# Performance work log

Hardware: AMD Instinct MI355X
Metric: run time of the kernel (lower is better)

Reference implementation:

```python
import jax, jax.numpy as jnp
import numpy as np

NUM_TOKENS = 2048
NUM_EXPERTS = 8
TOPK = 2
INTERMEDIATE = 2048
HIDDEN = 1024


def setup_inputs() -> dict:
    key = jax.random.key(0)
    k1, k2, k3 = jax.random.split(key, 3)
    intermediate_states = jax.random.normal(k1, (NUM_TOKENS * TOPK, INTERMEDIATE), dtype=jnp.float32)
    # per-expert down-projection, scaled like a typical init
    w = jax.random.normal(k2, (NUM_EXPERTS, INTERMEDIATE, HIDDEN), dtype=jnp.float32) / np.float32(np.sqrt(INTERMEDIATE))
    router_logits = jax.random.normal(k3, (NUM_TOKENS, NUM_EXPERTS), dtype=jnp.float32)
    return {"intermediate_states": intermediate_states, "w": w, "router_logits": router_logits}


def reference(intermediate_states, w, router_logits):
    T, E = router_logits.shape
    K = TOPK
    H = w.shape[-1]
    # Routing: softmax over experts, then top-k weights/ids (precompute_ctx.full_topk_weight/full_topk_ids)
    probs = jax.nn.softmax(router_logits, axis=-1)          # [T, E]
    topk_w, topk_ids = jax.lax.top_k(probs, K)              # [T, K]
    # Grouped expert GEMM: each (token, k) row is multiplied by its expert's weight.
    # Compute against all experts once, then gather the routed expert per row.
    out_all = jnp.einsum('ri,eih->reh', intermediate_states, w)   # [T*K, E, H]
    flat_ids = topk_ids.reshape(-1)                               # [T*K]
    routed = jnp.take_along_axis(out_all, flat_ids[:, None, None], axis=1)[:, 0, :]  # [T*K, H]
    # topk-weighted reduction over the K expert outputs per token
    out = (routed.reshape(T, K, H) * topk_w[..., None]).sum(axis=1)  # [T, H]
    # reduce-scatter across tensor-parallel ranks: with world_size=1 this is identity
    return out
```

## Files before the change

kernel.cpp:

```cpp
#include <hip/hip_runtime.h>

#define T_TOKENS 2048
#define N_EXPERTS 8
#define ROWS (T_TOKENS * 2)
#define I_DIM 2048
#define H_DIM 1024

#define M_TILE 64
#define N_TILE 128
#define BK 64
#define NSTEP (I_DIM / BK)

#define TP 68

typedef __bf16 bf16x8 __attribute__((ext_vector_type(8)));
typedef float f32x4 __attribute__((ext_vector_type(4)));
typedef unsigned int u32;
typedef u32 u32x4 __attribute__((ext_vector_type(4)));

__device__ inline void load_lds16(const void* g, void* l) {
    __builtin_amdgcn_global_load_lds(
        (const __attribute__((address_space(1))) void*)g,
        (__attribute__((address_space(3))) void*)l, 16, 0, 0);
}

__device__ inline u32 pack2(float a, float b) {
    union { __bf16 h[2]; u32 w; } u;
    u.h[0] = (__bf16)a; u.h[1] = (__bf16)b;
    return u.w;
}

__global__ __launch_bounds__(256) void prep_kernel(
    const float* __restrict__ w, const float* __restrict__ x,
    const float* __restrict__ logits,
    __bf16* __restrict__ wT, __bf16* __restrict__ xB,
    float* __restrict__ out, float* __restrict__ topk_w,
    int* __restrict__ cnt, int* __restrict__ rowlist) {
    const int b = blockIdx.x;
    const int t = threadIdx.x;
    if (b == 0) {
        __shared__ int lcnt[N_EXPERTS];
        if (t < N_EXPERTS) lcnt[t] = 0;
        __syncthreads();
#pragma unroll
        for (int i = 0; i < 8; ++i) {
            int tok = i * 256 + t;
            float l[8];
#pragma unroll
            for (int e = 0; e < 8; ++e) l[e] = logits[tok * 8 + e];
            float mx = l[0];
#pragma unroll
            for (int e = 1; e < 8; ++e) mx = fmaxf(mx, l[e]);
            float s = 0.f;
#pragma unroll
            for (int e = 0; e < 8; ++e) { l[e] = expf(l[e] - mx); s += l[e]; }
            float inv = 1.f / s;
            float v0 = -1.f, v1 = -1.f; int i0 = 0, i1 = 0;
#pragma unroll
            for (int e = 0; e < 8; ++e) {
                float p = l[e] * inv;
                if (p > v0)      { v1 = v0; i1 = i0; v0 = p; i0 = e; }
                else if (p > v1) { v1 = p; i1 = e; }
            }
            topk_w[2 * tok]     = v0;
            topk_w[2 * tok + 1] = v1;
            int p0 = atomicAdd(&lcnt[i0], 1); rowlist[i0 * ROWS + p0] = 2 * tok;
            int p1 = atomicAdd(&lcnt[i1], 1); rowlist[i1 * ROWS + p1] = 2 * tok + 1;
        }
        __syncthreads();
        if (t < N_EXPERTS) cnt[t] = lcnt[t];
    } else if (b < 2049) {
        const int bb = b - 1;
        __shared__ u32 tile[64 * TP];
        const int e = bb >> 8;
        const int k0 = ((bb >> 4) & 15) * 128;
        const int n0 = (bb & 15) * 64;
        const float* ws = w + (size_t)e * (I_DIM * H_DIM) + (size_t)k0 * H_DIM + n0;
#pragma unroll
        for (int i = 0; i < 4; ++i) {
            int kp = i * 16 + (t >> 4);
            int nq = (t & 15) * 4;
            const float* p = ws + (size_t)(2 * kp) * H_DIM + nq;
            f32x4 v0 = *(const f32x4*)p;
            f32x4 v1 = *(const f32x4*)(p + H_DIM);
            tile[(nq + 0) * TP + kp] = pack2(v0.x, v1.x);
            tile[(nq + 1) * TP + kp] = pack2(v0.y, v1.y);
            tile[(nq + 2) * TP + kp] = pack2(v0.z, v1.z);
            tile[(nq + 3) * TP + kp] = pack2(v0.w, v1.w);
        }
        __syncthreads();
        __bf16* wd = wT + (size_t)e * (H_DIM * I_DIM) + (size_t)n0 * I_DIM + k0;
#pragma unroll
        for (int i = 0; i < 4; ++i) {
            int n = i * 16 + (t >> 4);
            int c = t & 15;
            u32x4 r = *(const u32x4*)&tile[n * TP + 4 * c];
            *(u32x4*)(wd + (size_t)n * I_DIM + 8 * c) = r;
        }
    } else if (b < 4097) {
        size_t base = ((size_t)(b - 2049) * 256 + t) * 16;
        const f32x4* xs = (const f32x4*)(x + base);
        f32x4 v0 = xs[0], v1 = xs[1], v2 = xs[2], v3 = xs[3];
        bf16x8 o0 = { (__bf16)v0.x, (__bf16)v0.y, (__bf16)v0.z, (__bf16)v0.w,
                      (__bf16)v1.x, (__bf16)v1.y, (__bf16)v1.z, (__bf16)v1.w };
        bf16x8 o1 = { (__bf16)v2.x, (__bf16)v2.y, (__bf16)v2.z, (__bf16)v2.w,
                      (__bf16)v3.x, (__bf16)v3.y, (__bf16)v3.z, (__bf16)v3.w };
        *(bf16x8*)(xB + base) = o0;
        *(bf16x8*)(xB + base + 8) = o1;
    } else {
        size_t idx = (size_t)(b - 4097) * 256 + t;
        f32x4 z = (f32x4){0.f, 0.f, 0.f, 0.f};
        ((f32x4*)out)[2 * idx] = z;
        ((f32x4*)out)[2 * idx + 1] = z;
    }
}

__global__ __launch_bounds__(256, 3) void gemm_kernel(
    const __bf16* __restrict__ xB, const __bf16* __restrict__ wT,
    const int* __restrict__ cnt, const int* __restrict__ rowlist,
    const float* __restrict__ topk_w, float* __restrict__ out) {
    const int flat = blockIdx.x;
    const int e  = flat & 7;
    const int nt = (flat >> 3) & 7;
    const int mz = flat >> 6;
    const int cnt_e = cnt[e];
    const int m0 = mz * M_TILE;
    if (m0 >= cnt_e) return;
    const int n0 = nt * N_TILE;
    const int tid = threadIdx.x;
    const int lane = tid & 63;
    const int wave = tid >> 6;
    const int wm = wave & 1, wn = wave >> 1;

    __shared__ __bf16 As[2][M_TILE * BK];
    __shared__ __bf16 Bs[2][N_TILE * BK];

    const int* rl = rowlist + e * ROWS;

    const int lc = lane & 7;
    const int lr = lane >> 3;
    const int cg = lc ^ lr;

    int gm0 = m0 + 16 * wave + lr;
    int gm1 = gm0 + 8;
    if (gm0 >= cnt_e) gm0 = cnt_e - 1;
    if (gm1 >= cnt_e) gm1 = cnt_e - 1;
    const __bf16* asrc0 = xB + (size_t)rl[gm0] * I_DIM + cg * 8;
    const __bf16* asrc1 = xB + (size_t)rl[gm1] * I_DIM + cg * 8;
    const __bf16* wTe = wT + (size_t)e * (H_DIM * I_DIM);
    const __bf16* bsrc = wTe + (size_t)(n0 + 32 * wave + lr) * I_DIM + cg * 8;

    const int lm = lane & 15, lg = lane >> 4, sw = lm & 7;
    int offA[2][2], offB[2][4];
#pragma unroll
    for (int s = 0; s < 2; ++s) {
        int cs = (((s * 4) + lg) ^ sw) * 8;
#pragma unroll
        for (int mt = 0; mt < 2; ++mt)
            offA[s][mt] = (wm * 32 + mt * 16 + lm) * BK + cs;
#pragma unroll
        for (int nt2 = 0; nt2 < 4; ++nt2)
            offB[s][nt2] = (wn * 64 + nt2 * 16 + lm) * BK + cs;
    }

    f32x4 acc[2][4];
#pragma unroll
    for (int mt = 0; mt < 2; ++mt)
#pragma unroll
        for (int nt2 = 0; nt2 < 4; ++nt2)
            acc[mt][nt2] = (f32x4){0.f, 0.f, 0.f, 0.f};

#define STAGE(buf, koff)                                                  \
    do {                                                                  \
        load_lds16(asrc0 + (koff), &As[buf][wave * 1024]);                \
        load_lds16(asrc1 + (koff), &As[buf][wave * 1024 + 512]);          \
        load_lds16(bsrc + (koff),               &Bs[buf][wave * 2048]);   \
        load_lds16(bsrc +  8 * I_DIM + (koff),  &Bs[buf][wave * 2048 + 512]);  \
        load_lds16(bsrc + 16 * I_DIM + (koff),  &Bs[buf][wave * 2048 + 1024]); \
        load_lds16(bsrc + 24 * I_DIM + (koff),  &Bs[buf][wave * 2048 + 1536]); \
    } while (0)

    STAGE(0, 0);

    for (int t = 0; t < NSTEP; ++t) {
        const int cur = t & 1;
        if (t + 1 < NSTEP) {
            STAGE(cur ^ 1, (t + 1) * BK);
            asm volatile("s_waitcnt vmcnt(6)" ::: "memory");
        } else {
            asm volatile("s_waitcnt vmcnt(0)" ::: "memory");
        }
        __builtin_amdgcn_s_barrier();
        asm volatile("" ::: "memory");

        const __bf16* Ab = As[cur];
        const __bf16* Bb = Bs[cur];
#pragma unroll
        for (int s = 0; s < 2; ++s) {
            bf16x8 af[2], bfr[4];
#pragma unroll
            for (int f = 0; f < 2; ++f) af[f] = *(const bf16x8*)&Ab[offA[s][f]];
#pragma unroll
            for (int f = 0; f < 4; ++f) bfr[f] = *(const bf16x8*)&Bb[offB[s][f]];
#pragma unroll
            for (int mt = 0; mt < 2; ++mt)
#pragma unroll
                for (int nt2 = 0; nt2 < 4; ++nt2)
                    acc[mt][nt2] = __builtin_amdgcn_mfma_f32_16x16x32_bf16(
                        af[mt], bfr[nt2], acc[mt][nt2], 0, 0, 0);
        }
        asm volatile("" ::: "memory");
        __builtin_amdgcn_s_barrier();
    }
#undef STAGE

    const int lq = lane >> 4, ln = lane & 15;
#pragma unroll
    for (int mt = 0; mt < 2; ++mt) {
#pragma unroll
        for (int j = 0; j < 4; ++j) {
            int gm = m0 + wm * 32 + mt * 16 + lq * 4 + j;
            if (gm < cnt_e) {
                int row = rl[gm];
                float tw = topk_w[row];
                float* orow = out + (size_t)(row >> 1) * H_DIM + n0 + wn * 64 + ln;
#pragma unroll
                for (int nt2 = 0; nt2 < 4; ++nt2)
                    atomicAdd(&orow[nt2 * 16], acc[mt][nt2][j] * tw);
            }
        }
    }
}

extern "C" void kernel_launch(void* const* d_in, const int* in_sizes, int n_in,
                              void* d_out, int out_size, void* d_ws, size_t ws_size,
                              hipStream_t stream) {
    const float* x      = (const float*)d_in[0];
    const float* w      = (const float*)d_in[1];
    const float* logits = (const float*)d_in[2];
    float* out = (float*)d_out;

    char* ws = (char*)d_ws;
    float*  topk_w  = (float*)ws;
    int*    cnt     = (int*)(ws + 16384);
    int*    rowlist = (int*)(ws + 16384 + 128);
    __bf16* wT      = (__bf16*)(ws + 16384 + 128 + 131072);
    __bf16* xB      = (__bf16*)(ws + 16384 + 128 + 131072 + 33554432);

    prep_kernel<<<5121, 256, 0, stream>>>(w, x, logits, wT, xB, out, topk_w, cnt, rowlist);
    gemm_kernel<<<N_EXPERTS * (H_DIM / N_TILE) * (ROWS / M_TILE), 256, 0, stream>>>(
        xB, wT, cnt, rowlist, topk_w, out);
}
```

Baseline: 165.4 us.

## Double GEMM M-tile to 128 rows and interleave weight-transpose with activation-convert blocks

The GEMM M-tile grows from 64 to 128 rows. Each wave now stages four A row groups and keeps a 4x4 MFMA accumulator grid, which doubles reuse of each B tile loaded from LDS and halves the number of weight tiles fetched per routed row. Launch bounds drop from 3 to 2 blocks per CU to fit the extra registers, and the vmcnt wait is adjusted for the larger stage. The prep kernel also interleaves weight-transpose and activation-convert blocks (odd/even block ids) so both kinds of work are spread across CUs instead of running in sequence. Risks are lower occupancy, more wasted rows in partially filled tiles, and needing the host grid to match the new M-tile count.

```diff
diff --git a/kernel.cpp b/kernel.cpp
--- a/kernel.cpp
+++ b/kernel.cpp
@@ -6,7 +6,7 @@
 #define I_DIM 2048
 #define H_DIM 1024
 
-#define M_TILE 64
+#define M_TILE 128
 #define N_TILE 128
 #define BK 64
 #define NSTEP (I_DIM / BK)
@@ -69,8 +69,8 @@
         }
         __syncthreads();
         if (t < N_EXPERTS) cnt[t] = lcnt[t];
-    } else if (b < 2049) {
-        const int bb = b - 1;
+    } else if (b < 4097 && (b & 1)) {
+        const int bb = (b - 1) >> 1;
         __shared__ u32 tile[64 * TP];
         const int e = bb >> 8;
         const int k0 = ((bb >> 4) & 15) * 128;
@@ -98,7 +98,8 @@
             *(u32x4*)(wd + (size_t)n * I_DIM + 8 * c) = r;
         }
     } else if (b < 4097) {
-        size_t base = ((size_t)(b - 2049) * 256 + t) * 16;
+        const int cb = (b - 2) >> 1;
+        size_t base = ((size_t)cb * 256 + t) * 16;
         const f32x4* xs = (const f32x4*)(x + base);
         f32x4 v0 = xs[0], v1 = xs[1], v2 = xs[2], v3 = xs[3];
         bf16x8 o0 = { (__bf16)v0.x, (__bf16)v0.y, (__bf16)v0.z, (__bf16)v0.w,
@@ -115,7 +116,7 @@
     }
 }
 
-__global__ __launch_bounds__(256, 3) void gemm_kernel(
+__global__ __launch_bounds__(256, 2) void gemm_kernel(
     const __bf16* __restrict__ xB, const __bf16* __restrict__ wT,
     const int* __restrict__ cnt, const int* __restrict__ rowlist,
     const float* __restrict__ topk_w, float* __restrict__ out) {
@@ -141,39 +142,41 @@
     const int lr = lane >> 3;
     const int cg = lc ^ lr;
 
-    int gm0 = m0 + 16 * wave + lr;
-    int gm1 = gm0 + 8;
-    if (gm0 >= cnt_e) gm0 = cnt_e - 1;
-    if (gm1 >= cnt_e) gm1 = cnt_e - 1;
-    const __bf16* asrc0 = xB + (size_t)rl[gm0] * I_DIM + cg * 8;
-    const __bf16* asrc1 = xB + (size_t)rl[gm1] * I_DIM + cg * 8;
+    const __bf16* asrc[4];
+#pragma unroll
+    for (int i = 0; i < 4; ++i) {
+        int gm = m0 + 32 * wave + 8 * i + lr;
+        if (gm >= cnt_e) gm = cnt_e - 1;
+        asrc[i] = xB + (size_t)rl[gm] * I_DIM + cg * 8;
+    }
     const __bf16* wTe = wT + (size_t)e * (H_DIM * I_DIM);
     const __bf16* bsrc = wTe + (size_t)(n0 + 32 * wave + lr) * I_DIM + cg * 8;
 
     const int lm = lane & 15, lg = lane >> 4, sw = lm & 7;
-    int offA[2][2], offB[2][4];
+    int offA[2][4], offB[2][4];
 #pragma unroll
     for (int s = 0; s < 2; ++s) {
         int cs = (((s * 4) + lg) ^ sw) * 8;
 #pragma unroll
-        for (int mt = 0; mt < 2; ++mt)
-            offA[s][mt] = (wm * 32 + mt * 16 + lm) * BK + cs;
-#pragma unroll
-        for (int nt2 = 0; nt2 < 4; ++nt2)
-            offB[s][nt2] = (wn * 64 + nt2 * 16 + lm) * BK + cs;
-    }
-
-    f32x4 acc[2][4];
-#pragma unroll
-    for (int mt = 0; mt < 2; ++mt)
+        for (int f = 0; f < 4; ++f) {
+            offA[s][f] = (wm * 64 + f * 16 + lm) * BK + cs;
+            offB[s][f] = (wn * 64 + f * 16 + lm) * BK + cs;
+        }
+    }
+
+    f32x4 acc[4][4];
+#pragma unroll
+    for (int mt = 0; mt < 4; ++mt)
 #pragma unroll
         for (int nt2 = 0; nt2 < 4; ++nt2)
             acc[mt][nt2] = (f32x4){0.f, 0.f, 0.f, 0.f};
 
 #define STAGE(buf, koff)                                                  \
     do {                                                                  \
-        load_lds16(asrc0 + (koff), &As[buf][wave * 1024]);                \
-        load_lds16(asrc1 + (koff), &As[buf][wave * 1024 + 512]);          \
+        load_lds16(asrc[0] + (koff), &As[buf][wave * 2048]);              \
+        load_lds16(asrc[1] + (koff), &As[buf][wave * 2048 + 512]);        \
+        load_lds16(asrc[2] + (koff), &As[buf][wave * 2048 + 1024]);       \
+        load_lds16(asrc[3] + (koff), &As[buf][wave * 2048 + 1536]);       \
         load_lds16(bsrc + (koff),               &Bs[buf][wave * 2048]);   \
         load_lds16(bsrc +  8 * I_DIM + (koff),  &Bs[buf][wave * 2048 + 512]);  \
         load_lds16(bsrc + 16 * I_DIM + (koff),  &Bs[buf][wave * 2048 + 1024]); \
@@ -186,7 +189,7 @@
         const int cur = t & 1;
         if (t + 1 < NSTEP) {
             STAGE(cur ^ 1, (t + 1) * BK);
-            asm volatile("s_waitcnt vmcnt(6)" ::: "memory");
+            asm volatile("s_waitcnt vmcnt(8)" ::: "memory");
         } else {
             asm volatile("s_waitcnt vmcnt(0)" ::: "memory");
         }
@@ -197,13 +200,13 @@
         const __bf16* Bb = Bs[cur];
 #pragma unroll
         for (int s = 0; s < 2; ++s) {
-            bf16x8 af[2], bfr[4];
-#pragma unroll
-            for (int f = 0; f < 2; ++f) af[f] = *(const bf16x8*)&Ab[offA[s][f]];
+            bf16x8 af[4], bfr[4];
+#pragma unroll
+            for (int f = 0; f < 4; ++f) af[f] = *(const bf16x8*)&Ab[offA[s][f]];
 #pragma unroll
             for (int f = 0; f < 4; ++f) bfr[f] = *(const bf16x8*)&Bb[offB[s][f]];
 #pragma unroll
-            for (int mt = 0; mt < 2; ++mt)
+            for (int mt = 0; mt < 4; ++mt)
 #pragma unroll
                 for (int nt2 = 0; nt2 < 4; ++nt2)
                     acc[mt][nt2] = __builtin_amdgcn_mfma_f32_16x16x32_bf16(
@@ -216,10 +219,10 @@
 
     const int lq = lane >> 4, ln = lane & 15;
 #pragma unroll
-    for (int mt = 0; mt < 2; ++mt) {
+    for (int mt = 0; mt < 4; ++mt) {
 #pragma unroll
         for (int j = 0; j < 4; ++j) {
-            int gm = m0 + wm * 32 + mt * 16 + lq * 4 + j;
+            int gm = m0 + wm * 64 + mt * 16 + lq * 4 + j;
             if (gm < cnt_e) {
                 int row = rl[gm];
                 float tw = topk_w[row];
```

Result: slower. 176.1 us (+6.5%).

## Load A fragments directly to registers, stage only B in LDS

Applied to the files above, without the earlier changes.

The gathered activation rows are no longer staged through shared memory. Each wave loads its A MFMA fragments straight from global memory into registers, double-buffered across an unrolled-by-two k loop. Only the weight tile still goes through LDS, which reduces shared memory per block so occupancy can rise to 4 blocks. In exchange, waves sharing rows issue redundant global loads, the per-lane gather reads are less coalesced, and register pressure increases.

```diff
diff --git a/kernel.cpp b/kernel.cpp
--- a/kernel.cpp
+++ b/kernel.cpp
@@ -115,7 +115,7 @@
     }
 }
 
-__global__ __launch_bounds__(256, 3) void gemm_kernel(
+__global__ __launch_bounds__(256, 4) void gemm_kernel(
     const __bf16* __restrict__ xB, const __bf16* __restrict__ wT,
     const int* __restrict__ cnt, const int* __restrict__ rowlist,
     const float* __restrict__ topk_w, float* __restrict__ out) {
@@ -132,7 +132,6 @@
     const int wave = tid >> 6;
     const int wm = wave & 1, wn = wave >> 1;
 
-    __shared__ __bf16 As[2][M_TILE * BK];
     __shared__ __bf16 Bs[2][N_TILE * BK];
 
     const int* rl = rowlist + e * ROWS;
@@ -140,27 +139,22 @@
     const int lc = lane & 7;
     const int lr = lane >> 3;
     const int cg = lc ^ lr;
-
-    int gm0 = m0 + 16 * wave + lr;
-    int gm1 = gm0 + 8;
-    if (gm0 >= cnt_e) gm0 = cnt_e - 1;
-    if (gm1 >= cnt_e) gm1 = cnt_e - 1;
-    const __bf16* asrc0 = xB + (size_t)rl[gm0] * I_DIM + cg * 8;
-    const __bf16* asrc1 = xB + (size_t)rl[gm1] * I_DIM + cg * 8;
     const __bf16* wTe = wT + (size_t)e * (H_DIM * I_DIM);
     const __bf16* bsrc = wTe + (size_t)(n0 + 32 * wave + lr) * I_DIM + cg * 8;
 
     const int lm = lane & 15, lg = lane >> 4, sw = lm & 7;
-    int offA[2][2], offB[2][4];
+    int gmA0 = m0 + wm * 32 + lm;       if (gmA0 >= cnt_e) gmA0 = cnt_e - 1;
+    int gmA1 = m0 + wm * 32 + 16 + lm;  if (gmA1 >= cnt_e) gmA1 = cnt_e - 1;
+    const __bf16* abase0 = xB + (size_t)rl[gmA0] * I_DIM + lg * 8;
+    const __bf16* abase1 = xB + (size_t)rl[gmA1] * I_DIM + lg * 8;
+
+    int offB[2][4];
 #pragma unroll
     for (int s = 0; s < 2; ++s) {
         int cs = (((s * 4) + lg) ^ sw) * 8;
 #pragma unroll
-        for (int mt = 0; mt < 2; ++mt)
-            offA[s][mt] = (wm * 32 + mt * 16 + lm) * BK + cs;
-#pragma unroll
-        for (int nt2 = 0; nt2 < 4; ++nt2)
-            offB[s][nt2] = (wn * 64 + nt2 * 16 + lm) * BK + cs;
+        for (int f = 0; f < 4; ++f)
+            offB[s][f] = (wn * 64 + f * 16 + lm) * BK + cs;
     }
 
     f32x4 acc[2][4];
@@ -170,49 +164,84 @@
         for (int nt2 = 0; nt2 < 4; ++nt2)
             acc[mt][nt2] = (f32x4){0.f, 0.f, 0.f, 0.f};
 
-#define STAGE(buf, koff)                                                  \
-    do {                                                                  \
-        load_lds16(asrc0 + (koff), &As[buf][wave * 1024]);                \
-        load_lds16(asrc1 + (koff), &As[buf][wave * 1024 + 512]);          \
-        load_lds16(bsrc + (koff),               &Bs[buf][wave * 2048]);   \
+#define STAGE_B(buf, koff)                                                     \
+    do {                                                                       \
+        load_lds16(bsrc + (koff),               &Bs[buf][wave * 2048]);        \
         load_lds16(bsrc +  8 * I_DIM + (koff),  &Bs[buf][wave * 2048 + 512]);  \
         load_lds16(bsrc + 16 * I_DIM + (koff),  &Bs[buf][wave * 2048 + 1024]); \
         load_lds16(bsrc + 24 * I_DIM + (koff),  &Bs[buf][wave * 2048 + 1536]); \
     } while (0)
 
-    STAGE(0, 0);
-
-    for (int t = 0; t < NSTEP; ++t) {
-        const int cur = t & 1;
-        if (t + 1 < NSTEP) {
-            STAGE(cur ^ 1, (t + 1) * BK);
-            asm volatile("s_waitcnt vmcnt(6)" ::: "memory");
+#define ALOAD(d00, d01, d10, d11, koff)                                        \
+    do {                                                                       \
+        d00 = *(const bf16x8*)(abase0 + (koff));                   \
+        d01 = *(const bf16x8*)(abase0 + (koff) + 32);              \
+        d10 = *(const bf16x8*)(abase1 + (koff));                   \
+        d11 = *(const bf16x8*)(abase1 + (koff) + 32);              \
+    } while (0)
+
+#define COMPUTE(buf, a00, a01, a10, a11)                                       \
+    do {                                                                       \
+        const __bf16* Bb = Bs[buf];                                            \
+        bf16x8 b0, b1, b2, b3;                                                 \
+        b0 = *(const bf16x8*)&Bb[offB[0][0]];                                  \
+        b1 = *(const bf16x8*)&Bb[offB[0][1]];                                  \
+        b2 = *(const bf16x8*)&Bb[offB[0][2]];                                  \
+        b3 = *(const bf16x8*)&Bb[offB[0][3]];                                  \
+        acc[0][0] = __builtin_amdgcn_mfma_f32_16x16x32_bf16(a00, b0, acc[0][0], 0, 0, 0); \
+        acc[0][1] = __builtin_amdgcn_mfma_f32_16x16x32_bf16(a00, b1, acc[0][1], 0, 0, 0); \
+        acc[0][2] = __builtin_amdgcn_mfma_f32_16x16x32_bf16(a00, b2, acc[0][2], 0, 0, 0); \
+        acc[0][3] = __builtin_amdgcn_mfma_f32_16x16x32_bf16(a00, b3, acc[0][3], 0, 0, 0); \
+        acc[1][0] = __builtin_amdgcn_mfma_f32_16x16x32_bf16(a10, b0, acc[1][0], 0, 0, 0); \
+        acc[1][1] = __builtin_amdgcn_mfma_f32_16x16x32_bf16(a10, b1, acc[1][1], 0, 0, 0); \
+        acc[1][2] = __builtin_amdgcn_mfma_f32_16x16x32_bf16(a10, b2, acc[1][2], 0, 0, 0); \
+        acc[1][3] = __builtin_amdgcn_mfma_f32_16x16x32_bf16(a10, b3, acc[1][3], 0, 0, 0); \
+        b0 = *(const bf16x8*)&Bb[offB[1][0]];                                  \
+        b1 = *(const bf16x8*)&Bb[offB[1][1]];                                  \
+        b2 = *(const bf16x8*)&Bb[offB[1][2]];                                  \
+        b3 = *(const bf16x8*)&Bb[offB[1][3]];                                  \
+        acc[0][0] = __builtin_amdgcn_mfma_f32_16x16x32_bf16(a01, b0, acc[0][0], 0, 0, 0); \
+        acc[0][1] = __builtin_amdgcn_mfma_f32_16x16x32_bf16(a01, b1, acc[0][1], 0, 0, 0); \
+        acc[0][2] = __builtin_amdgcn_mfma_f32_16x16x32_bf16(a01, b2, acc[0][2], 0, 0, 0); \
+        acc[0][3] = __builtin_amdgcn_mfma_f32_16x16x32_bf16(a01, b3, acc[0][3], 0, 0, 0); \
+        acc[1][0] = __builtin_amdgcn_mfma_f32_16x16x32_bf16(a11, b0, acc[1][0], 0, 0, 0); \
+        acc[1][1] = __builtin_amdgcn_mfma_f32_16x16x32_bf16(a11, b1, acc[1][1], 0, 0, 0); \
+        acc[1][2] = __builtin_amdgcn_mfma_f32_16x16x32_bf16(a11, b2, acc[1][2], 0, 0, 0); \
+        acc[1][3] = __builtin_amdgcn_mfma_f32_16x16x32_bf16(a11, b3, acc[1][3], 0, 0, 0); \
+    } while (0)
+
+    bf16x8 aX00, aX01, aX10, aX11;
+    bf16x8 aY00, aY01, aY10, aY11;
+
+    STAGE_B(0, 0);
+    ALOAD(aX00, aX01, aX10, aX11, 0);
+
+    for (int t = 0; t < NSTEP; t += 2) {
+        STAGE_B(1, (t + 1) * BK);
+        ALOAD(aY00, aY01, aY10, aY11, (t + 1) * BK);
+        asm volatile("s_waitcnt vmcnt(8)" ::: "memory");
+        __builtin_amdgcn_s_barrier();
+        asm volatile("" ::: "memory");
+        COMPUTE(0, aX00, aX01, aX10, aX11);
+        asm volatile("" ::: "memory");
+        __builtin_amdgcn_s_barrier();
+
+        if (t + 2 < NSTEP) {
+            STAGE_B(0, (t + 2) * BK);
+            ALOAD(aX00, aX01, aX10, aX11, (t + 2) * BK);
+            asm volatile("s_waitcnt vmcnt(8)" ::: "memory");
         } else {
             asm volatile("s_waitcnt vmcnt(0)" ::: "memory");
         }
         __builtin_amdgcn_s_barrier();
         asm volatile("" ::: "memory");
-
-        const __bf16* Ab = As[cur];
-        const __bf16* Bb = Bs[cur];
-#pragma unroll
-        for (int s = 0; s < 2; ++s) {
-            bf16x8 af[2], bfr[4];
-#pragma unroll
-            for (int f = 0; f < 2; ++f) af[f] = *(const bf16x8*)&Ab[offA[s][f]];
-#pragma unroll
-            for (int f = 0; f < 4; ++f) bfr[f] = *(const bf16x8*)&Bb[offB[s][f]];
-#pragma unroll
-            for (int mt = 0; mt < 2; ++mt)
-#pragma unroll
-                for (int nt2 = 0; nt2 < 4; ++nt2)
-                    acc[mt][nt2] = __builtin_amdgcn_mfma_f32_16x16x32_bf16(
-                        af[mt], bfr[nt2], acc[mt][nt2], 0, 0, 0);
-        }
-        asm volatile("" ::: "memory");
-        __builtin_amdgcn_s_barrier();
-    }
-#undef STAGE
+        COMPUTE(1, aY00, aY01, aY10, aY11);
+        asm volatile("" ::: "memory");
+        __builtin_amdgcn_s_barrier();
+    }
+#undef STAGE_B
+#undef ALOAD
+#undef COMPUTE
 
     const int lq = lane >> 4, ln = lane & 15;
 #pragma unroll
```

Measured after the change: 186.6 us. 12.8% more time.
